# Optimization experiments

Hardware: AMD Instinct MI355X
Metric: run time of the kernel (lower is better)

## Reference

```python
import jax, jax.numpy as jnp
from jax import lax
import numpy as np

C_IN, C_OUT = 8, 16
H_IN = W_IN = 56
S = 28  # input_size: side of the original network input (symbolic coeff map)
K = 3
STRIDE = (1, 1)
PAD = ((1, 1), (1, 1))
DIL = (1, 1)


def setup_inputs() -> dict:
    key = jax.random.key(0)
    k = jax.random.split(key, 6)
    return {
        "lx_in": jax.random.normal(k[0], (C_IN, H_IN, W_IN, S, S), jnp.float32),
        "ux_in": jax.random.normal(k[1], (C_IN, H_IN, W_IN, S, S), jnp.float32),
        "lc_in": jax.random.normal(k[2], (C_IN, H_IN, W_IN), jnp.float32),
        "uc_in": jax.random.normal(k[3], (C_IN, H_IN, W_IN), jnp.float32),
        "weight": jax.random.normal(k[4], (C_OUT, C_IN, K, K), jnp.float32),
        "bias": jax.random.normal(k[5], (C_OUT,), jnp.float32),
    }


def _conv_sym(x, w):
    # x: (Cin, H, W, S, S) symbolic coefficient maps -> fold (S,S) into conv batch
    Cin, Hh, Ww, S1, S2 = x.shape
    xb = x.reshape(Cin, Hh, Ww, S1 * S2).transpose(3, 0, 1, 2)  # (S*S, Cin, H, W)
    y = lax.conv_general_dilated(xb, w, STRIDE, PAD, rhs_dilation=DIL)
    _, Cout, Ho, Wo = y.shape
    return y.transpose(1, 2, 3, 0).reshape(Cout, Ho, Wo, S1, S2)


def _conv_const(c, w):
    # c: (Cin, H, W) constant offsets -> batch of 1
    y = lax.conv_general_dilated(c[None], w, STRIDE, PAD, rhs_dilation=DIL)
    return y[0]  # (Cout, Ho, Wo)


def reference(lx_in, ux_in, lc_in, uc_in, weight, bias):
    # sign-split weights: strictly positive / strictly negative parts (zeros drop out)
    w_pos = jnp.where(weight > 0, weight, 0.0)
    w_neg = jnp.where(weight < 0, weight, 0.0)
    # Interval-bound conv: lower bound mixes lower coeffs through w_pos and
    # upper coeffs through w_neg (and symmetrically for the upper bound).
    lx_out = _conv_sym(lx_in, w_pos) + _conv_sym(ux_in, w_neg)
    ux_out = _conv_sym(ux_in, w_pos) + _conv_sym(lx_in, w_neg)
    lc_out = _conv_const(lc_in, w_pos) + _conv_const(uc_in, w_neg) + bias[:, None, None]
    uc_out = _conv_const(uc_in, w_pos) + _conv_const(lc_in, w_neg) + bias[:, None, None]
    return (lx_out, ux_out, lc_out, uc_out)
```

## Files before the change

kernel.cpp:

```cpp
#include <hip/hip_runtime.h>

#define CIN   8
#define COUT  16
#define HH    56
#define WW    56
#define SS    784
#define PLANE (HH * WW * SS)
#define ROW   (WW * SS)
#define NF4   (HH * WW * (SS / 4))
#define SYM_OUT_SZ (COUT * PLANE)

__global__ __launch_bounds__(256) void ibp_conv_sym(
    const float* __restrict__ lx, const float* __restrict__ ux,
    const float* __restrict__ wgt,
    float* __restrict__ lx_out, float* __restrict__ ux_out)
{
    __shared__ float2 wsh[72][COUT];
    const int tid = threadIdx.x;
    for (int i = tid; i < 72 * COUT; i += 256) {
        int tap = i >> 4, co = i & 15;
        int ci = tap / 9, r = tap - ci * 9;
        int dh = r / 3, dw = r - dh * 3;
        float w = wgt[((co * CIN + ci) * 3 + dh) * 3 + dw];
        wsh[tap][co] = make_float2(0.5f * w, 0.5f * fabsf(w));
    }
    __syncthreads();

    const int gi  = blockIdx.x * 256 + tid;
    const int pix = gi / 196;
    const int j4  = gi - pix * 196;
    const int h   = pix / WW;
    const int w   = pix - h * WW;
    (void)j4;

    const float* bl0 = lx + (size_t)gi * 4;
    const float* bu0 = ux + (size_t)gi * 4;

    float4 A[COUT], B[COUT];
    #pragma unroll
    for (int co = 0; co < COUT; ++co) {
        A[co] = make_float4(0.f, 0.f, 0.f, 0.f);
        B[co] = make_float4(0.f, 0.f, 0.f, 0.f);
    }

    for (int ci = 0; ci < CIN; ++ci) {
        const float* bl = bl0 + ci * PLANE;
        const float* bu = bu0 + ci * PLANE;
        #pragma unroll
        for (int dh = 0; dh < 3; ++dh) {
            const int ih = h + dh - 1;
            const bool vh = (unsigned)ih < (unsigned)HH;
            #pragma unroll
            for (int dw = 0; dw < 3; ++dw) {
                const int iw = w + dw - 1;
                const bool ok = vh && ((unsigned)iw < (unsigned)WW);
                const int off = (dh - 1) * ROW + (dw - 1) * SS;
                float4 lv = make_float4(0.f, 0.f, 0.f, 0.f);
                float4 uv = make_float4(0.f, 0.f, 0.f, 0.f);
                if (ok) {
                    lv = *(const float4*)(bl + off);
                    uv = *(const float4*)(bu + off);
                }
                const float sx = lv.x + uv.x, sy = lv.y + uv.y,
                            sz = lv.z + uv.z, sw = lv.w + uv.w;
                const float dx = lv.x - uv.x, dy = lv.y - uv.y,
                            dz = lv.z - uv.z, dwv = lv.w - uv.w;
                const int tap = ci * 9 + dh * 3 + dw;
                #pragma unroll
                for (int co = 0; co < COUT; ++co) {
                    const float2 wp = wsh[tap][co];
                    A[co].x += wp.x * sx;  A[co].y += wp.x * sy;
                    A[co].z += wp.x * sz;  A[co].w += wp.x * sw;
                    B[co].x += wp.y * dx;  B[co].y += wp.y * dy;
                    B[co].z += wp.y * dz;  B[co].w += wp.y * dwv;
                }
            }
        }
    }

    #pragma unroll
    for (int co = 0; co < COUT; ++co) {
        float4 lo, uo;
        lo.x = A[co].x + B[co].x;  uo.x = A[co].x - B[co].x;
        lo.y = A[co].y + B[co].y;  uo.y = A[co].y - B[co].y;
        lo.z = A[co].z + B[co].z;  uo.z = A[co].z - B[co].z;
        lo.w = A[co].w + B[co].w;  uo.w = A[co].w - B[co].w;
        *(float4*)(lx_out + (size_t)co * PLANE + (size_t)gi * 4) = lo;
        *(float4*)(ux_out + (size_t)co * PLANE + (size_t)gi * 4) = uo;
    }
}

__global__ __launch_bounds__(256) void ibp_conv_const(
    const float* __restrict__ lc, const float* __restrict__ uc,
    const float* __restrict__ wgt, const float* __restrict__ bias,
    float* __restrict__ lc_out, float* __restrict__ uc_out)
{
    const int idx = blockIdx.x * 256 + threadIdx.x;
    if (idx >= COUT * HH * WW) return;
    const int co  = idx / (HH * WW);
    const int pix = idx - co * (HH * WW);
    const int h = pix / WW, w = pix - (pix / WW) * WW;

    float Aa = 0.f, Bb = 0.f;
    for (int ci = 0; ci < CIN; ++ci) {
        #pragma unroll
        for (int dh = 0; dh < 3; ++dh) {
            const int ih = h + dh - 1;
            if ((unsigned)ih >= (unsigned)HH) continue;
            #pragma unroll
            for (int dw = 0; dw < 3; ++dw) {
                const int iw = w + dw - 1;
                if ((unsigned)iw >= (unsigned)WW) continue;
                const float l = lc[(ci * HH + ih) * WW + iw];
                const float u = uc[(ci * HH + ih) * WW + iw];
                const float wv = wgt[((co * CIN + ci) * 3 + dh) * 3 + dw];
                Aa += wv * (l + u);
                Bb += fabsf(wv) * (l - u);
            }
        }
    }
    const float b = bias[co];
    lc_out[idx] = 0.5f * (Aa + Bb) + b;
    uc_out[idx] = 0.5f * (Aa - Bb) + b;
}

extern "C" void kernel_launch(void* const* d_in, const int* in_sizes, int n_in,
                              void* d_out, int out_size, void* d_ws, size_t ws_size,
                              hipStream_t stream) {
    const float* lx   = (const float*)d_in[0];
    const float* ux   = (const float*)d_in[1];
    const float* lc   = (const float*)d_in[2];
    const float* uc   = (const float*)d_in[3];
    const float* wgt  = (const float*)d_in[4];
    const float* bias = (const float*)d_in[5];

    float* out    = (float*)d_out;
    float* lx_out = out;
    float* ux_out = out + (size_t)SYM_OUT_SZ;
    float* lc_out = out + (size_t)2 * SYM_OUT_SZ;
    float* uc_out = lc_out + COUT * HH * WW;

    ibp_conv_sym<<<NF4 / 256, 256, 0, stream>>>(lx, ux, wgt, lx_out, ux_out);

    const int nconst = COUT * HH * WW;
    ibp_conv_const<<<(nconst + 255) / 256, 256, 0, stream>>>(
        lc, uc, wgt, bias, lc_out, uc_out);
}
```

Baseline: 646.9 us.

## Use packed FMA, scalar-cached weights, and band-swizzled block order in symbolic conv

Result: slower. 1.432 ms (+121.4%).

```diff
diff --git a/kernel.cpp b/kernel.cpp
--- a/kernel.cpp
+++ b/kernel.cpp
@@ -10,37 +10,59 @@
 #define NF4   (HH * WW * (SS / 4))
 #define SYM_OUT_SZ (COUT * PLANE)
 
-__global__ __launch_bounds__(256) void ibp_conv_sym(
+typedef float f32x2 __attribute__((ext_vector_type(2)));
+typedef float f32x4 __attribute__((ext_vector_type(4)));
+
+#if defined(__has_builtin)
+#if __has_builtin(__builtin_elementwise_fma)
+#define PK_FMA(a, b, c) __builtin_elementwise_fma((a), (b), (c))
+#endif
+#endif
+#ifndef PK_FMA
+#define PK_FMA(a, b, c) ((a) * (b) + (c))
+#endif
+
+__global__ __launch_bounds__(256) void ibp_prep_w(
+    const float* __restrict__ wgt, float* __restrict__ wtr)
+{
+    const int i = blockIdx.x * 256 + threadIdx.x;
+    if (i >= 72 * 16) return;
+    const int tap = i >> 4, co = i & 15;
+    const int ci = tap / 9, r = tap - ci * 9;
+    const float w = wgt[(co * CIN + ci) * 9 + r];
+    wtr[tap * 32 + co]      = 0.5f * w;
+    wtr[tap * 32 + 16 + co] = 0.5f * fabsf(w);
+}
+
+__global__ __launch_bounds__(256, 3) void ibp_conv_sym(
     const float* __restrict__ lx, const float* __restrict__ ux,
-    const float* __restrict__ wgt,
+    const float* __restrict__ wtr,
     float* __restrict__ lx_out, float* __restrict__ ux_out)
 {
-    __shared__ float2 wsh[72][COUT];
     const int tid = threadIdx.x;
-    for (int i = tid; i < 72 * COUT; i += 256) {
-        int tap = i >> 4, co = i & 15;
-        int ci = tap / 9, r = tap - ci * 9;
-        int dh = r / 3, dw = r - dh * 3;
-        float w = wgt[((co * CIN + ci) * 3 + dh) * 3 + dw];
-        wsh[tap][co] = make_float2(0.5f * w, 0.5f * fabsf(w));
-    }
-    __syncthreads();
+    const int b   = blockIdx.x;
+    const int vblk = (b < 2400) ? ((b & 7) * 300 + (b >> 3)) : b;
+    const int gv   = vblk * 256 + tid;
 
-    const int gi  = blockIdx.x * 256 + tid;
-    const int pix = gi / 196;
-    const int j4  = gi - pix * 196;
-    const int h   = pix / WW;
-    const int w   = pix - h * WW;
-    (void)j4;
+    const int j4   = gv % 196;
+    const int t    = gv / 196;
+    const int wi   = t & 7;
+    const int hb   = t >> 3;
+    const int h    = hb % 56;
+    const int band = hb / 56;
+    const int w    = band * 8 + wi;
 
-    const float* bl0 = lx + (size_t)gi * 4;
-    const float* bu0 = ux + (size_t)gi * 4;
+    const int pix  = h * WW + w;
+    const int base = pix * SS + j4 * 4;
 
-    float4 A[COUT], B[COUT];
+    const float* bl0 = lx + base;
+    const float* bu0 = ux + base;
+
+    f32x2 A0[COUT], A1[COUT], B0[COUT], B1[COUT];
     #pragma unroll
     for (int co = 0; co < COUT; ++co) {
-        A[co] = make_float4(0.f, 0.f, 0.f, 0.f);
-        B[co] = make_float4(0.f, 0.f, 0.f, 0.f);
+        A0[co] = (f32x2)0.f; A1[co] = (f32x2)0.f;
+        B0[co] = (f32x2)0.f; B1[co] = (f32x2)0.f;
     }
 
     for (int ci = 0; ci < CIN; ++ci) {
@@ -55,24 +77,30 @@
                 const int iw = w + dw - 1;
                 const bool ok = vh && ((unsigned)iw < (unsigned)WW);
                 const int off = (dh - 1) * ROW + (dw - 1) * SS;
-                float4 lv = make_float4(0.f, 0.f, 0.f, 0.f);
-                float4 uv = make_float4(0.f, 0.f, 0.f, 0.f);
+                f32x4 lv = (f32x4)0.f, uv = (f32x4)0.f;
                 if (ok) {
-                    lv = *(const float4*)(bl + off);
-                    uv = *(const float4*)(bu + off);
+                    lv = *(const f32x4*)(bl + off);
+                    uv = *(const f32x4*)(bu + off);
                 }
-                const float sx = lv.x + uv.x, sy = lv.y + uv.y,
-                            sz = lv.z + uv.z, sw = lv.w + uv.w;
-                const float dx = lv.x - uv.x, dy = lv.y - uv.y,
-                            dz = lv.z - uv.z, dwv = lv.w - uv.w;
+                const f32x4 s = lv + uv;
+                const f32x4 d = lv - uv;
+                const f32x2 s01 = __builtin_shufflevector(s, s, 0, 1);
+                const f32x2 s23 = __builtin_shufflevector(s, s, 2, 3);
+                const f32x2 d01 = __builtin_shufflevector(d, d, 0, 1);
+                const f32x2 d23 = __builtin_shufflevector(d, d, 2, 3);
+
                 const int tap = ci * 9 + dh * 3 + dw;
+                const float* wp = wtr + tap * 32;
                 #pragma unroll
                 for (int co = 0; co < COUT; ++co) {
-                    const float2 wp = wsh[tap][co];
-                    A[co].x += wp.x * sx;  A[co].y += wp.x * sy;
-                    A[co].z += wp.x * sz;  A[co].w += wp.x * sw;
-                    B[co].x += wp.y * dx;  B[co].y += wp.y * dy;
-                    B[co].z += wp.y * dz;  B[co].w += wp.y * dwv;
+                    const float wa = wp[co];
+                    const float wb = wp[16 + co];
+                    const f32x2 wa2 = {wa, wa};
+                    const f32x2 wb2 = {wb, wb};
+                    A0[co] = PK_FMA(wa2, s01, A0[co]);
+                    A1[co] = PK_FMA(wa2, s23, A1[co]);
+                    B0[co] = PK_FMA(wb2, d01, B0[co]);
+                    B1[co] = PK_FMA(wb2, d23, B1[co]);
                 }
             }
         }
@@ -80,13 +108,12 @@
 
     #pragma unroll
     for (int co = 0; co < COUT; ++co) {
-        float4 lo, uo;
-        lo.x = A[co].x + B[co].x;  uo.x = A[co].x - B[co].x;
-        lo.y = A[co].y + B[co].y;  uo.y = A[co].y - B[co].y;
-        lo.z = A[co].z + B[co].z;  uo.z = A[co].z - B[co].z;
-        lo.w = A[co].w + B[co].w;  uo.w = A[co].w - B[co].w;
-        *(float4*)(lx_out + (size_t)co * PLANE + (size_t)gi * 4) = lo;
-        *(float4*)(ux_out + (size_t)co * PLANE + (size_t)gi * 4) = uo;
+        const f32x4 a = __builtin_shufflevector(A0[co], A1[co], 0, 1, 2, 3);
+        const f32x4 bb = __builtin_shufflevector(B0[co], B1[co], 0, 1, 2, 3);
+        const f32x4 lo = a + bb;
+        const f32x4 uo = a - bb;
+        *(f32x4*)(lx_out + (size_t)co * PLANE + base) = lo;
+        *(f32x4*)(ux_out + (size_t)co * PLANE + base) = uo;
     }
 }
 
@@ -140,7 +167,11 @@
     float* lc_out = out + (size_t)2 * SYM_OUT_SZ;
     float* uc_out = lc_out + COUT * HH * WW;
 
-    ibp_conv_sym<<<NF4 / 256, 256, 0, stream>>>(lx, ux, wgt, lx_out, ux_out);
+    float* wtr = (float*)d_ws;
+
+    ibp_prep_w<<<(72 * 16 + 255) / 256, 256, 0, stream>>>(wgt, wtr);
+
+    ibp_conv_sym<<<NF4 / 256, 256, 0, stream>>>(lx, ux, wtr, lx_out, ux_out);
 
     const int nconst = COUT * HH * WW;
     ibp_conv_const<<<(nconst + 255) / 256, 256, 0, stream>>>(
```
